# Kernel tuning notes

Measured on AMD Instinct MI355X. Metric: run time of the kernel, lower is better.

Reference implementation:

```python
import jax, jax.numpy as jnp
import numpy as np

N, E, G = 100000, 1600000, 512
D_IN, D_H, D_OUT = 128, 128, 1
EPS = 1e-5


def _gcn_conv(x, W, b, src, dst, n):
    # PyG GCNConv: h = x @ W, add self-loops, symmetric-normalized sum aggregation, bias after.
    h = x @ W
    loop = jnp.arange(n)
    s = jnp.concatenate([src, loop])
    d = jnp.concatenate([dst, loop])
    deg = jax.ops.segment_sum(jnp.ones(s.shape[0], dtype=h.dtype), d, num_segments=n)
    dinv = jnp.where(deg > 0, jax.lax.rsqrt(deg), 0.0)
    norm = dinv[s] * dinv[d]  # [E+N]
    out = jax.ops.segment_sum(h[s] * norm[:, None], d, num_segments=n)
    return out + b


def _bn(x, g, b, m, v):
    # eval-mode BatchNorm1d
    return (x - m) * jax.lax.rsqrt(v + EPS) * g + b


def setup_inputs() -> dict:
    key = jax.random.key(0)
    ks = jax.random.split(key, 24)
    x = jax.random.normal(ks[0], (N, D_IN), dtype=jnp.float32)
    edge_index = jax.random.randint(ks[1], (2, E), 0, N, dtype=jnp.int64)
    batch = (jnp.arange(N, dtype=jnp.int64) * G) // N  # sorted, all graphs non-empty
    inp = {"x": x, "edge_index": edge_index, "batch": batch}
    dims = [(D_IN, D_H), (D_H, D_H), (D_H, D_H)]
    for i, (din, dout) in enumerate(dims):
        sc = 1.0 / np.sqrt(din)
        inp[f"W{i}"] = jax.random.normal(ks[2 + 4 * i], (din, dout), dtype=jnp.float32) * sc
        inp[f"cb{i}"] = jnp.zeros((dout,), dtype=jnp.float32)
        inp[f"g{i}"] = jnp.ones((dout,), dtype=jnp.float32)
        inp[f"bt{i}"] = jnp.zeros((dout,), dtype=jnp.float32)
        inp[f"m{i}"] = jax.random.normal(ks[3 + 4 * i], (dout,), dtype=jnp.float32) * 0.1
        inp[f"v{i}"] = jax.random.uniform(ks[4 + 4 * i], (dout,), dtype=jnp.float32, minval=0.5, maxval=1.5)
    inp["L1w"] = jax.random.normal(ks[15], (2 * D_H, D_H), dtype=jnp.float32) / np.sqrt(2 * D_H)
    inp["L1b"] = jnp.zeros((D_H,), dtype=jnp.float32)
    inp["L2w"] = jax.random.normal(ks[16], (D_H, D_H // 2), dtype=jnp.float32) / np.sqrt(D_H)
    inp["L2b"] = jnp.zeros((D_H // 2,), dtype=jnp.float32)
    inp["L3w"] = jax.random.normal(ks[17], (D_H // 2, D_OUT), dtype=jnp.float32) / np.sqrt(D_H // 2)
    inp["L3b"] = jnp.zeros((D_OUT,), dtype=jnp.float32)
    return inp


def reference(x, edge_index, batch,
              W0, cb0, g0, bt0, m0, v0,
              W1, cb1, g1, bt1, m1, v1,
              W2, cb2, g2, bt2, m2, v2,
              L1w, L1b, L2w, L2b, L3w, L3b):
    src, dst = edge_index[0], edge_index[1]
    Ws = [W0, W1, W2]
    cbs = [cb0, cb1, cb2]
    bns = [(g0, bt0, m0, v0), (g1, bt1, m1, v1), (g2, bt2, m2, v2)]
    for i in range(3):
        x_prev = x
        x = _gcn_conv(x, Ws[i], cbs[i], src, dst, N)
        x = jax.nn.relu(_bn(x, *bns[i]))
        # dropout is identity in eval mode
        if i > 0:
            x = x + x_prev  # residual (shapes match for i > 0)
    ones = jnp.ones((N,), dtype=x.dtype)
    cnt = jax.ops.segment_sum(ones, batch, num_segments=G)[:, None]
    x_mean = jax.ops.segment_sum(x, batch, num_segments=G) / cnt
    x_max = jax.ops.segment_max(x, batch, num_segments=G)
    h = jnp.concatenate([x_mean, x_max], axis=1)  # [G, 2*D_H]
    h = jax.nn.relu(h @ L1w + L1b)
    h = jax.nn.relu(h @ L2w + L2b)
    return h @ L3w + L3b  # [G, 1]
```

## Files before the change

### kernel.cpp

```cpp
#include <hip/hip_runtime.h>
#include <math.h>

#define DH 128
#define EPSB 1e-5f
#define MAXB 832
#define BCAP 3072

typedef __attribute__((ext_vector_type(8))) short short8;
typedef __attribute__((ext_vector_type(4))) float f32x4;

static __device__ __forceinline__ unsigned short f2bf(float f) {
    unsigned u = __float_as_uint(f);
    u += 0x7fffu + ((u >> 16) & 1u);
    return (unsigned short)(u >> 16);
}
static __device__ __forceinline__ float bf2f(unsigned short h) {
    return __uint_as_float(((unsigned)h) << 16);
}


__launch_bounds__(256)
__global__ void k_bucketA(const int* __restrict__ src, const int* __restrict__ dst,
                          int* __restrict__ gcur, int* __restrict__ bbuf,
                          const int* __restrict__ batch, int* __restrict__ starts,
                          int E, int NB, int chunk, int N, int G)
{
    __shared__ int cnt[MAXB];
    __shared__ int base[MAXB];
    const int t = threadIdx.x;

    for (int i = blockIdx.x * 256 + t; i < N; i += gridDim.x * 256) {
        int b = batch[i];
        if (i == 0) { starts[0] = 0; starts[G] = N; }
        else if (batch[i - 1] != b) starts[b] = i;
    }

    for (int i = t; i < NB; i += 256) cnt[i] = 0;
    __syncthreads();
    const int e0 = blockIdx.x * chunk;
    const int e1 = min(E, e0 + chunk);
    for (int e = e0 + t; e < e1; e += 256)
        atomicAdd(&cnt[dst[e] >> 7], 1);
    __syncthreads();
    for (int i = t; i < NB; i += 256) {
        int c = cnt[i];
        base[i] = (c > 0) ? atomicAdd(&gcur[i], c) : 0;
        cnt[i] = 0;
    }
    __syncthreads();
    for (int e = e0 + t; e < e1; e += 256) {
        int d = dst[e];
        int b = d >> 7;
        int o = base[b] + atomicAdd(&cnt[b], 1);
        if (o < BCAP) bbuf[(size_t)b * BCAP + o] = (src[e] << 7) | (d & 127);
    }
}

__launch_bounds__(1024)
__global__ void k_bgscan(const int* __restrict__ gcur, int* __restrict__ bbase,
                         int* __restrict__ rowptr, int NB, int N, int E)
{
    __shared__ int s[1024];
    int t = threadIdx.x;
    int v = (t < NB) ? min(gcur[t], BCAP) : 0;
    s[t] = v;
    __syncthreads();
    for (int off = 1; off < 1024; off <<= 1) {
        int u = (t >= off) ? s[t - off] : 0;
        __syncthreads();
        s[t] += u;
        __syncthreads();
    }
    if (t < NB) bbase[t] = s[t] - v;
    if (t == 0) rowptr[N] = E;
}

__launch_bounds__(256)
__global__ void k_bfinal(const int* __restrict__ gcur, const int* __restrict__ bbase,
                         const int* __restrict__ bbuf, int* __restrict__ rowptr,
                         float* __restrict__ dinv, int* __restrict__ csr_src, int N)
{
    __shared__ int ebuf[BCAP];
    __shared__ int dcnt[128];
    __shared__ int sp[128];
    const int b = blockIdx.x, t = threadIdx.x;
    const int c = min(gcur[b], BCAP);
    const int base = bbase[b];
    const int* p = bbuf + (size_t)b * BCAP;
    for (int i = t; i < c; i += 256) ebuf[i] = p[i];
    if (t < 128) dcnt[t] = 0;
    __syncthreads();
    for (int i = t; i < c; i += 256) atomicAdd(&dcnt[ebuf[i] & 127], 1);
    __syncthreads();
    if (t < 128) sp[t] = dcnt[t];
    __syncthreads();
    for (int off = 1; off < 128; off <<= 1) {
        int u = (t < 128 && t >= off) ? sp[t - off] : 0;
        __syncthreads();
        if (t < 128) sp[t] += u;
        __syncthreads();
    }
    if (t < 128) {
        sp[t] -= dcnt[t];
        int d = b * 128 + t;
        if (d < N) {
            rowptr[d] = base + sp[t];
            dinv[d] = rsqrtf((float)(dcnt[t] + 1));
        }
        dcnt[t] = 0;
    }
    __syncthreads();
    for (int i = t; i < c; i += 256) {
        int e = ebuf[i];
        int dl = e & 127;
        int o = atomicAdd(&dcnt[dl], 1);
        csr_src[base + sp[dl] + o] = e >> 7;
    }
}


__global__ void k_wfrag(const float* __restrict__ W0, const float* __restrict__ W1,
                        const float* __restrict__ W2, unsigned short* __restrict__ Wf0) {
    int fid = blockIdx.x * 4 + (threadIdx.x >> 6);
    int lane = threadIdx.x & 63;
    int l = fid >> 6;
    int f = fid & 63;
    const float* W = (l == 0) ? W0 : (l == 1) ? W1 : W2;
    unsigned short* Wf = Wf0 + (size_t)l * 32768;
    int nt = f & 3, s = (f >> 2) & 3, p = (f >> 4) & 1, nh = f >> 5;
    int n = nh * 64 + nt * 16 + (lane & 15);
    int kbase = s * 32 + (lane >> 4) * 8;
    unsigned short o[8];
#pragma unroll
    for (int j = 0; j < 8; ++j) {
        float w = W[(size_t)(kbase + j) * DH + n];
        unsigned short h = f2bf(w);
        o[j] = p ? f2bf(w - bf2f(h)) : h;
    }
    unsigned short* d = Wf + (size_t)f * 512 + lane * 8;
    *(ushort4*)d       = make_ushort4(o[0], o[1], o[2], o[3]);
    *(ushort4*)(d + 4) = make_ushort4(o[4], o[5], o[6], o[7]);
}


#define LDA0 132

__launch_bounds__(256)
__global__ void k_gemm0(const float* __restrict__ X,
                        const unsigned short* __restrict__ Wf,
                        const float* __restrict__ dinv,
                        unsigned short* __restrict__ hs, int N)
{
    __shared__ float As[64 * LDA0];

    const int tid  = threadIdx.x;
    const int lane = tid & 63, wave = tid >> 6;
    const int mh = wave >> 1, nh = wave & 1;
    const int rowBase = blockIdx.x * 64;
    const int r15 = lane & 15, quad = lane >> 4;

    {
        const float4* gp = (const float4*)(X + (size_t)rowBase * DH);
#pragma unroll
        for (int it = 0; it < 8; ++it) {
            int idx = it * 256 + tid;
            int grow = idx >> 5, gcol = idx & 31;
            float4 v = make_float4(0.f, 0.f, 0.f, 0.f);
            if (rowBase + grow < N) v = gp[idx];
            *(float4*)(As + grow * LDA0 + gcol * 4) = v;
        }
    }
    __syncthreads();

    f32x4 acc[2][4];
#pragma unroll
    for (int mt = 0; mt < 2; ++mt)
#pragma unroll
        for (int nt = 0; nt < 4; ++nt)
            acc[mt][nt] = (f32x4){0.f, 0.f, 0.f, 0.f};

#pragma unroll
    for (int s = 0; s < 4; ++s) {
        short8 wfh[4], wfl[4];
#pragma unroll
        for (int nt = 0; nt < 4; ++nt) {
            wfh[nt] = *(const short8*)(Wf + ((((nh * 2 + 0) * 4 + s) * 4 + nt) * 512) + lane * 8);
            wfl[nt] = *(const short8*)(Wf + ((((nh * 2 + 1) * 4 + s) * 4 + nt) * 512) + lane * 8);
        }
#pragma unroll
        for (int mt = 0; mt < 2; ++mt) {
            const float* ap = As + (mh * 32 + mt * 16 + r15) * LDA0 + s * 32 + quad * 8;
            short8 ah, al;
#pragma unroll
            for (int j = 0; j < 8; ++j) {
                float v = ap[j];
                unsigned short h = f2bf(v);
                ah[j] = (short)h;
                al[j] = (short)f2bf(v - bf2f(h));
            }
#pragma unroll
            for (int nt = 0; nt < 4; ++nt) {
                acc[mt][nt] = __builtin_amdgcn_mfma_f32_16x16x32_bf16(ah, wfh[nt], acc[mt][nt], 0, 0, 0);
                acc[mt][nt] = __builtin_amdgcn_mfma_f32_16x16x32_bf16(ah, wfl[nt], acc[mt][nt], 0, 0, 0);
                acc[mt][nt] = __builtin_amdgcn_mfma_f32_16x16x32_bf16(al, wfh[nt], acc[mt][nt], 0, 0, 0);
            }
        }
    }

#pragma unroll
    for (int mt = 0; mt < 2; ++mt) {
        int rl = mh * 32 + mt * 16 + quad * 4;
#pragma unroll
        for (int reg = 0; reg < 4; ++reg) {
            int row = rowBase + rl + reg;
            if (row < N) {
                float sc = dinv[row];
#pragma unroll
                for (int nt = 0; nt < 4; ++nt)
                    hs[(size_t)row * DH + nh * 64 + nt * 16 + r15] = f2bf(acc[mt][nt][reg] * sc);
            }
        }
    }
}


#define LDAP 136

__launch_bounds__(256)
__global__ void k_gemm_pl(const unsigned short* __restrict__ Xh,
                          const unsigned short* __restrict__ Xl,
                          const unsigned short* __restrict__ Wf,
                          const float* __restrict__ dinv,
                          unsigned short* __restrict__ hs, int N)
{
    __shared__ unsigned short Ah[64 * LDAP];
    __shared__ unsigned short Al[64 * LDAP];

    const int tid  = threadIdx.x;
    const int lane = tid & 63, wave = tid >> 6;
    const int mh = wave >> 1, nh = wave & 1;
    const int rowBase = blockIdx.x * 64;
    const int r15 = lane & 15, quad = lane >> 4;

    {
        const uint4* gh = (const uint4*)(Xh + (size_t)rowBase * DH);
        const uint4* gl = (const uint4*)(Xl + (size_t)rowBase * DH);
#pragma unroll
        for (int it = 0; it < 4; ++it) {
            int idx = it * 256 + tid;
            int grow = idx >> 4, gcol8 = (idx & 15) * 8;
            uint4 vh = make_uint4(0, 0, 0, 0), vl = make_uint4(0, 0, 0, 0);
            if (rowBase + grow < N) { vh = gh[idx]; vl = gl[idx]; }
            *(uint4*)(Ah + grow * LDAP + gcol8) = vh;
            *(uint4*)(Al + grow * LDAP + gcol8) = vl;
        }
    }
    __syncthreads();

    f32x4 acc[2][4];
#pragma unroll
    for (int mt = 0; mt < 2; ++mt)
#pragma unroll
        for (int nt = 0; nt < 4; ++nt)
            acc[mt][nt] = (f32x4){0.f, 0.f, 0.f, 0.f};

#pragma unroll
    for (int s = 0; s < 4; ++s) {
        short8 wfh[4], wfl[4];
#pragma unroll
        for (int nt = 0; nt < 4; ++nt) {
            wfh[nt] = *(const short8*)(Wf + ((((nh * 2 + 0) * 4 + s) * 4 + nt) * 512) + lane * 8);
            wfl[nt] = *(const short8*)(Wf + ((((nh * 2 + 1) * 4 + s) * 4 + nt) * 512) + lane * 8);
        }
#pragma unroll
        for (int mt = 0; mt < 2; ++mt) {
            int arow = mh * 32 + mt * 16 + r15;
            short8 ah = *(const short8*)(Ah + arow * LDAP + s * 32 + quad * 8);
            short8 al = *(const short8*)(Al + arow * LDAP + s * 32 + quad * 8);
#pragma unroll
            for (int nt = 0; nt < 4; ++nt) {
                acc[mt][nt] = __builtin_amdgcn_mfma_f32_16x16x32_bf16(ah, wfh[nt], acc[mt][nt], 0, 0, 0);
                acc[mt][nt] = __builtin_amdgcn_mfma_f32_16x16x32_bf16(ah, wfl[nt], acc[mt][nt], 0, 0, 0);
                acc[mt][nt] = __builtin_amdgcn_mfma_f32_16x16x32_bf16(al, wfh[nt], acc[mt][nt], 0, 0, 0);
            }
        }
    }

#pragma unroll
    for (int mt = 0; mt < 2; ++mt) {
        int rl = mh * 32 + mt * 16 + quad * 4;
#pragma unroll
        for (int reg = 0; reg < 4; ++reg) {
            int row = rowBase + rl + reg;
            if (row < N) {
                float sc = dinv[row];
#pragma unroll
                for (int nt = 0; nt < 4; ++nt)
                    hs[(size_t)row * DH + nh * 64 + nt * 16 + r15] = f2bf(acc[mt][nt][reg] * sc);
            }
        }
    }
}


__launch_bounds__(256)
__global__ void k_gather(const unsigned short* __restrict__ hs, const int* __restrict__ rowptr,
                         const int* __restrict__ csr_src, const float* __restrict__ dinv,
                         const float* __restrict__ cb, const float* __restrict__ bm,
                         const float* __restrict__ bv, const float* __restrict__ bg,
                         const float* __restrict__ bb,
                         const unsigned short* __restrict__ ph,
                         const unsigned short* __restrict__ pl,
                         unsigned short* __restrict__ oh,
                         unsigned short* __restrict__ ol,
                         int N)
{
    const int node = (blockIdx.x * blockDim.x + threadIdx.x) >> 5;
    const int lh = threadIdx.x & 31;
    if (node >= N) return;
    const int f = lh * 4;
    const int e0 = rowptr[node], e1 = rowptr[node + 1];

    ushort4 su = *(const ushort4*)(hs + (size_t)node * DH + f);
    float a0 = bf2f(su.x), a1 = bf2f(su.y), a2 = bf2f(su.z), a3 = bf2f(su.w);

    for (int base = e0; base < e1; base += 32) {
        int cnt = e1 - base; if (cnt > 32) cnt = 32;
        int idx = (lh < cnt) ? csr_src[base + lh] : 0;
        int i = 0;
        for (; i + 4 <= cnt; i += 4) {
            int s0 = __shfl(idx, i,     32), s1 = __shfl(idx, i + 1, 32);
            int s2 = __shfl(idx, i + 2, 32), s3 = __shfl(idx, i + 3, 32);
            ushort4 v0 = *(const ushort4*)(hs + (size_t)s0 * DH + f);
            ushort4 v1 = *(const ushort4*)(hs + (size_t)s1 * DH + f);
            ushort4 v2 = *(const ushort4*)(hs + (size_t)s2 * DH + f);
            ushort4 v3 = *(const ushort4*)(hs + (size_t)s3 * DH + f);
            a0 += (bf2f(v0.x) + bf2f(v1.x)) + (bf2f(v2.x) + bf2f(v3.x));
            a1 += (bf2f(v0.y) + bf2f(v1.y)) + (bf2f(v2.y) + bf2f(v3.y));
            a2 += (bf2f(v0.z) + bf2f(v1.z)) + (bf2f(v2.z) + bf2f(v3.z));
            a3 += (bf2f(v0.w) + bf2f(v1.w)) + (bf2f(v2.w) + bf2f(v3.w));
        }
        for (; i < cnt; ++i) {
            int s = __shfl(idx, i, 32);
            ushort4 v = *(const ushort4*)(hs + (size_t)s * DH + f);
            a0 += bf2f(v.x); a1 += bf2f(v.y); a2 += bf2f(v.z); a3 += bf2f(v.w);
        }
    }

    const float sc = dinv[node];
    const float4 vcb = *(const float4*)(cb + f);
    const float4 vbm = *(const float4*)(bm + f);
    const float4 vbv = *(const float4*)(bv + f);
    const float4 vbg = *(const float4*)(bg + f);
    const float4 vbb = *(const float4*)(bb + f);
    float o0 = (a0 * sc + vcb.x - vbm.x) * rsqrtf(vbv.x + EPSB) * vbg.x + vbb.x;
    float o1 = (a1 * sc + vcb.y - vbm.y) * rsqrtf(vbv.y + EPSB) * vbg.y + vbb.y;
    float o2 = (a2 * sc + vcb.z - vbm.z) * rsqrtf(vbv.z + EPSB) * vbg.z + vbb.z;
    float o3 = (a3 * sc + vcb.w - vbm.w) * rsqrtf(vbv.w + EPSB) * vbg.w + vbb.w;
    o0 = fmaxf(o0, 0.f); o1 = fmaxf(o1, 0.f); o2 = fmaxf(o2, 0.f); o3 = fmaxf(o3, 0.f);
    if (ph) {
        ushort4 hv = *(const ushort4*)(ph + (size_t)node * DH + f);
        ushort4 lv = *(const ushort4*)(pl + (size_t)node * DH + f);
        o0 += bf2f(hv.x) + bf2f(lv.x);
        o1 += bf2f(hv.y) + bf2f(lv.y);
        o2 += bf2f(hv.z) + bf2f(lv.z);
        o3 += bf2f(hv.w) + bf2f(lv.w);
    }
    unsigned short h0 = f2bf(o0), h1 = f2bf(o1), h2 = f2bf(o2), h3 = f2bf(o3);
    *(ushort4*)(oh + (size_t)node * DH + f) = make_ushort4(h0, h1, h2, h3);
    *(ushort4*)(ol + (size_t)node * DH + f) =
        make_ushort4(f2bf(o0 - bf2f(h0)), f2bf(o1 - bf2f(h1)),
                     f2bf(o2 - bf2f(h2)), f2bf(o3 - bf2f(h3)));
}


__launch_bounds__(128)
__global__ void k_pool_mlp(const unsigned short* __restrict__ xh,
                           const unsigned short* __restrict__ xl,
                           const int* __restrict__ starts,
                           const float* __restrict__ L1w, const float* __restrict__ L1b,
                           const float* __restrict__ L2w, const float* __restrict__ L2b,
                           const float* __restrict__ L3w, const float* __restrict__ L3b,
                           float* __restrict__ out)
{
    int g = blockIdx.x, t = threadIdx.x;
    int s0 = starts[g], s1 = starts[g + 1];
    const int half = t >> 6;
    const int tc = t & 63;
    const int fc = tc * 2;

    float sA = 0.f, sB = 0.f;
    float mA = -INFINITY, mB = -INFINITY;
    for (int i = s0 + half; i < s1; i += 2) {
        unsigned hv = *(const unsigned*)(xh + (size_t)i * DH + fc);
        unsigned lv = *(const unsigned*)(xl + (size_t)i * DH + fc);
        float vA = bf2f((unsigned short)hv) + bf2f((unsigned short)lv);
        float vB = bf2f((unsigned short)(hv >> 16)) + bf2f((unsigned short)(lv >> 16));
        sA += vA; sB += vB;
        mA = fmaxf(mA, vA); mB = fmaxf(mB, vB);
    }

    __shared__ float ps[2][128];
    __shared__ float pm[2][128];
    ps[half][fc] = sA; ps[half][fc + 1] = sB;
    pm[half][fc] = mA; pm[half][fc + 1] = mB;
    __syncthreads();

    __shared__ float h[256];
    if (half == 0) {
        float inv = 1.f / (float)(s1 - s0);
        h[fc]     = (ps[0][fc]     + ps[1][fc])     * inv;
        h[fc + 1] = (ps[0][fc + 1] + ps[1][fc + 1]) * inv;
        h[128 + fc]     = fmaxf(pm[0][fc],     pm[1][fc]);
        h[128 + fc + 1] = fmaxf(pm[0][fc + 1], pm[1][fc + 1]);
    }
    __syncthreads();

    float a = L1b[t];
    for (int k = 0; k < 256; ++k) a += h[k] * L1w[k * DH + t];
    __shared__ float h1[128];
    h1[t] = fmaxf(a, 0.f);
    __syncthreads();

    __shared__ float h2[64];
    if (t < 64) {
        float a2 = L2b[t];
        for (int k = 0; k < 128; ++k) a2 += h1[k] * L2w[k * 64 + t];
        h2[t] = fmaxf(a2, 0.f);
    }
    __syncthreads();

    if (t < 64) {
        float p = h2[t] * L3w[t];
#pragma unroll
        for (int off = 32; off > 0; off >>= 1) p += __shfl_down(p, off, 64);
        if (t == 0) out[g] = p + L3b[0];
    }
}


static inline char* align16(char* p) {
    return (char*)(((uintptr_t)p + 15) & ~(uintptr_t)15);
}

extern "C" void kernel_launch(void* const* d_in, const int* in_sizes, int n_in,
                              void* d_out, int out_size, void* d_ws, size_t ws_size,
                              hipStream_t stream)
{
    const float* x     = (const float*)d_in[0];
    const int*   ei    = (const int*)d_in[1];
    const int*   batch = (const int*)d_in[2];
    const int N = in_sizes[0] / DH;
    const int E = in_sizes[1] / 2;
    const int G = out_size;
    const int* src = ei;
    const int* dst = ei + E;

    const float* W[3]  = {(const float*)d_in[3],  (const float*)d_in[9],  (const float*)d_in[15]};
    const float* cb[3] = {(const float*)d_in[4],  (const float*)d_in[10], (const float*)d_in[16]};
    const float* bg[3] = {(const float*)d_in[5],  (const float*)d_in[11], (const float*)d_in[17]};
    const float* bt[3] = {(const float*)d_in[6],  (const float*)d_in[12], (const float*)d_in[18]};
    const float* bm[3] = {(const float*)d_in[7],  (const float*)d_in[13], (const float*)d_in[19]};
    const float* bv[3] = {(const float*)d_in[8],  (const float*)d_in[14], (const float*)d_in[20]};
    const float* L1w = (const float*)d_in[21]; const float* L1b = (const float*)d_in[22];
    const float* L2w = (const float*)d_in[23]; const float* L2b = (const float*)d_in[24];
    const float* L3w = (const float*)d_in[25]; const float* L3b = (const float*)d_in[26];

    char* wsp = (char*)d_ws;
    size_t planeB = (size_t)N * DH * sizeof(unsigned short);
    unsigned short* HS  = (unsigned short*)wsp; wsp += planeB;
    unsigned short* AH  = (unsigned short*)wsp; wsp += planeB;
    unsigned short* AL  = (unsigned short*)wsp; wsp += planeB;
    unsigned short* BH  = (unsigned short*)wsp; wsp += planeB;
    unsigned short* BL  = (unsigned short*)wsp; wsp += planeB;
    unsigned short* Wfrag = (unsigned short*)wsp; wsp += 3 * 65536;
    float* dinv   = (float*)wsp; wsp += (size_t)N * sizeof(float);
    int*   rowptr = (int*)wsp;   wsp = align16(wsp + (size_t)(N + 1) * sizeof(int));
    int*   csr_src= (int*)wsp;   wsp += (size_t)E * sizeof(int);
    int*   starts = (int*)wsp;   wsp = align16(wsp + (size_t)(G + 1) * sizeof(int));
    int*   gcur   = (int*)wsp;   wsp = align16(wsp + (size_t)MAXB * sizeof(int));
    int*   bbase  = (int*)wsp;   wsp = align16(wsp + (size_t)MAXB * sizeof(int));
    int*   bbuf   = (int*)wsp;   wsp += (size_t)MAXB * BCAP * sizeof(int);

    const int NB = (N + 127) >> 7;
    const int nblkA = 128;
    const int chunk = (E + nblkA - 1) / nblkA;

    hipMemsetAsync(gcur, 0, (size_t)NB * sizeof(int), stream);
    k_bucketA<<<nblkA, 256, 0, stream>>>(src, dst, gcur, bbuf, batch, starts,
                                         E, NB, chunk, N, G);
    k_bgscan <<<1, 1024, 0, stream>>>(gcur, bbase, rowptr, NB, N, E);
    k_bfinal <<<NB, 256, 0, stream>>>(gcur, bbase, bbuf, rowptr, dinv, csr_src, N);
    k_wfrag  <<<48, 256, 0, stream>>>(W[0], W[1], W[2], Wfrag);

    int gemmGrid = (N + 63) / 64;
    int gathGrid = ((size_t)N * 32 + 255) / 256;

    k_gemm0<<<gemmGrid, 256, 0, stream>>>(x, Wfrag, dinv, HS, N);
    k_gather<<<gathGrid, 256, 0, stream>>>(HS, rowptr, csr_src, dinv,
                                           cb[0], bm[0], bv[0], bg[0], bt[0],
                                           nullptr, nullptr, AH, AL, N);
    k_gemm_pl<<<gemmGrid, 256, 0, stream>>>(AH, AL, Wfrag + 32768, dinv, HS, N);
    k_gather<<<gathGrid, 256, 0, stream>>>(HS, rowptr, csr_src, dinv,
                                           cb[1], bm[1], bv[1], bg[1], bt[1],
                                           AH, AL, BH, BL, N);
    k_gemm_pl<<<gemmGrid, 256, 0, stream>>>(BH, BL, Wfrag + 65536, dinv, HS, N);
    k_gather<<<gathGrid, 256, 0, stream>>>(HS, rowptr, csr_src, dinv,
                                           cb[2], bm[2], bv[2], bg[2], bt[2],
                                           BH, BL, AH, AL, N);

    k_pool_mlp<<<G, 128, 0, stream>>>(AH, AL, starts, L1w, L1b, L2w, L2b, L3w, L3b,
                                      (float*)d_out);
}
```

Baseline: 530.1 us.

## Widen gather loads to 16 bytes per lane, use more pool threads and bucket blocks

The gather kernel now assigns 16 lanes per node, each loading 8 bf16 features with one 128-bit load instead of 32 lanes with 64-bit loads. This halves the load instructions and shuffles per edge and lets each wave process twice as many nodes. The pool/MLP kernel moves from 128 to 256 threads so four row groups reduce each graph, and the bucketing kernel launches 512 blocks instead of 128. Each lane now holds more accumulator registers, and the shorter edge chunks of 16 mean more loop iterations per node.

Result: faster. 507.4 us (-4.3%).

```diff
diff --git a/kernel.cpp b/kernel.cpp
--- a/kernel.cpp
+++ b/kernel.cpp
@@ -17,6 +17,8 @@
 static __device__ __forceinline__ float bf2f(unsigned short h) {
     return __uint_as_float(((unsigned)h) << 16);
 }
+static __device__ __forceinline__ float blo(unsigned u) { return __uint_as_float(u << 16); }
+static __device__ __forceinline__ float bhi(unsigned u) { return __uint_as_float(u & 0xFFFF0000u); }
 
 
 __launch_bounds__(256)
@@ -315,66 +317,84 @@
                          unsigned short* __restrict__ ol,
                          int N)
 {
-    const int node = (blockIdx.x * blockDim.x + threadIdx.x) >> 5;
-    const int lh = threadIdx.x & 31;
+    const int node = (blockIdx.x * blockDim.x + threadIdx.x) >> 4;
+    const int lh = threadIdx.x & 15;
     if (node >= N) return;
-    const int f = lh * 4;
+    const int f = lh * 8;
     const int e0 = rowptr[node], e1 = rowptr[node + 1];
 
-    ushort4 su = *(const ushort4*)(hs + (size_t)node * DH + f);
-    float a0 = bf2f(su.x), a1 = bf2f(su.y), a2 = bf2f(su.z), a3 = bf2f(su.w);
-
-    for (int base = e0; base < e1; base += 32) {
-        int cnt = e1 - base; if (cnt > 32) cnt = 32;
+    const uint4* hsv = (const uint4*)hs;
+    float a[8];
+    {
+        uint4 sv = hsv[(size_t)node * 16 + lh];
+        a[0] = blo(sv.x); a[1] = bhi(sv.x); a[2] = blo(sv.y); a[3] = bhi(sv.y);
+        a[4] = blo(sv.z); a[5] = bhi(sv.z); a[6] = blo(sv.w); a[7] = bhi(sv.w);
+    }
+
+    for (int base = e0; base < e1; base += 16) {
+        int cnt = e1 - base; if (cnt > 16) cnt = 16;
         int idx = (lh < cnt) ? csr_src[base + lh] : 0;
         int i = 0;
         for (; i + 4 <= cnt; i += 4) {
-            int s0 = __shfl(idx, i,     32), s1 = __shfl(idx, i + 1, 32);
-            int s2 = __shfl(idx, i + 2, 32), s3 = __shfl(idx, i + 3, 32);
-            ushort4 v0 = *(const ushort4*)(hs + (size_t)s0 * DH + f);
-            ushort4 v1 = *(const ushort4*)(hs + (size_t)s1 * DH + f);
-            ushort4 v2 = *(const ushort4*)(hs + (size_t)s2 * DH + f);
-            ushort4 v3 = *(const ushort4*)(hs + (size_t)s3 * DH + f);
-            a0 += (bf2f(v0.x) + bf2f(v1.x)) + (bf2f(v2.x) + bf2f(v3.x));
-            a1 += (bf2f(v0.y) + bf2f(v1.y)) + (bf2f(v2.y) + bf2f(v3.y));
-            a2 += (bf2f(v0.z) + bf2f(v1.z)) + (bf2f(v2.z) + bf2f(v3.z));
-            a3 += (bf2f(v0.w) + bf2f(v1.w)) + (bf2f(v2.w) + bf2f(v3.w));
+            int s0 = __shfl(idx, i,     16), s1 = __shfl(idx, i + 1, 16);
+            int s2 = __shfl(idx, i + 2, 16), s3 = __shfl(idx, i + 3, 16);
+            uint4 v0 = hsv[(size_t)s0 * 16 + lh];
+            uint4 v1 = hsv[(size_t)s1 * 16 + lh];
+            uint4 v2 = hsv[(size_t)s2 * 16 + lh];
+            uint4 v3 = hsv[(size_t)s3 * 16 + lh];
+            a[0] += (blo(v0.x) + blo(v1.x)) + (blo(v2.x) + blo(v3.x));
+            a[1] += (bhi(v0.x) + bhi(v1.x)) + (bhi(v2.x) + bhi(v3.x));
+            a[2] += (blo(v0.y) + blo(v1.y)) + (blo(v2.y) + blo(v3.y));
+            a[3] += (bhi(v0.y) + bhi(v1.y)) + (bhi(v2.y) + bhi(v3.y));
+            a[4] += (blo(v0.z) + blo(v1.z)) + (blo(v2.z) + blo(v3.z));
+            a[5] += (bhi(v0.z) + bhi(v1.z)) + (bhi(v2.z) + bhi(v3.z));
+            a[6] += (blo(v0.w) + blo(v1.w)) + (blo(v2.w) + blo(v3.w));
+            a[7] += (bhi(v0.w) + bhi(v1.w)) + (bhi(v2.w) + bhi(v3.w));
         }
         for (; i < cnt; ++i) {
-            int s = __shfl(idx, i, 32);
-            ushort4 v = *(const ushort4*)(hs + (size_t)s * DH + f);
-            a0 += bf2f(v.x); a1 += bf2f(v.y); a2 += bf2f(v.z); a3 += bf2f(v.w);
+            int s = __shfl(idx, i, 16);
+            uint4 v = hsv[(size_t)s * 16 + lh];
+            a[0] += blo(v.x); a[1] += bhi(v.x); a[2] += blo(v.y); a[3] += bhi(v.y);
+            a[4] += blo(v.z); a[5] += bhi(v.z); a[6] += blo(v.w); a[7] += bhi(v.w);
         }
     }
 
     const float sc = dinv[node];
-    const float4 vcb = *(const float4*)(cb + f);
-    const float4 vbm = *(const float4*)(bm + f);
-    const float4 vbv = *(const float4*)(bv + f);
-    const float4 vbg = *(const float4*)(bg + f);
-    const float4 vbb = *(const float4*)(bb + f);
-    float o0 = (a0 * sc + vcb.x - vbm.x) * rsqrtf(vbv.x + EPSB) * vbg.x + vbb.x;
-    float o1 = (a1 * sc + vcb.y - vbm.y) * rsqrtf(vbv.y + EPSB) * vbg.y + vbb.y;
-    float o2 = (a2 * sc + vcb.z - vbm.z) * rsqrtf(vbv.z + EPSB) * vbg.z + vbb.z;
-    float o3 = (a3 * sc + vcb.w - vbm.w) * rsqrtf(vbv.w + EPSB) * vbg.w + vbb.w;
-    o0 = fmaxf(o0, 0.f); o1 = fmaxf(o1, 0.f); o2 = fmaxf(o2, 0.f); o3 = fmaxf(o3, 0.f);
+    float cbv[8], bmv[8], bvv[8], bgv[8], bbv[8];
+    *(float4*)cbv = *(const float4*)(cb + f); *(float4*)(cbv + 4) = *(const float4*)(cb + f + 4);
+    *(float4*)bmv = *(const float4*)(bm + f); *(float4*)(bmv + 4) = *(const float4*)(bm + f + 4);
+    *(float4*)bvv = *(const float4*)(bv + f); *(float4*)(bvv + 4) = *(const float4*)(bv + f + 4);
+    *(float4*)bgv = *(const float4*)(bg + f); *(float4*)(bgv + 4) = *(const float4*)(bg + f + 4);
+    *(float4*)bbv = *(const float4*)(bb + f); *(float4*)(bbv + 4) = *(const float4*)(bb + f + 4);
+
+    float o[8];
+#pragma unroll
+    for (int j = 0; j < 8; ++j) {
+        float v = (a[j] * sc + cbv[j] - bmv[j]) * rsqrtf(bvv[j] + EPSB) * bgv[j] + bbv[j];
+        o[j] = fmaxf(v, 0.f);
+    }
     if (ph) {
-        ushort4 hv = *(const ushort4*)(ph + (size_t)node * DH + f);
-        ushort4 lv = *(const ushort4*)(pl + (size_t)node * DH + f);
-        o0 += bf2f(hv.x) + bf2f(lv.x);
-        o1 += bf2f(hv.y) + bf2f(lv.y);
-        o2 += bf2f(hv.z) + bf2f(lv.z);
-        o3 += bf2f(hv.w) + bf2f(lv.w);
-    }
-    unsigned short h0 = f2bf(o0), h1 = f2bf(o1), h2 = f2bf(o2), h3 = f2bf(o3);
-    *(ushort4*)(oh + (size_t)node * DH + f) = make_ushort4(h0, h1, h2, h3);
-    *(ushort4*)(ol + (size_t)node * DH + f) =
-        make_ushort4(f2bf(o0 - bf2f(h0)), f2bf(o1 - bf2f(h1)),
-                     f2bf(o2 - bf2f(h2)), f2bf(o3 - bf2f(h3)));
-}
-
-
-__launch_bounds__(128)
+        uint4 hv = *(const uint4*)(ph + (size_t)node * DH + f);
+        uint4 lv = *(const uint4*)(pl + (size_t)node * DH + f);
+        o[0] += blo(hv.x) + blo(lv.x); o[1] += bhi(hv.x) + bhi(lv.x);
+        o[2] += blo(hv.y) + blo(lv.y); o[3] += bhi(hv.y) + bhi(lv.y);
+        o[4] += blo(hv.z) + blo(lv.z); o[5] += bhi(hv.z) + bhi(lv.z);
+        o[6] += blo(hv.w) + blo(lv.w); o[7] += bhi(hv.w) + bhi(lv.w);
+    }
+    unsigned hw[4], lw[4];
+#pragma unroll
+    for (int p = 0; p < 4; ++p) {
+        unsigned short hA = f2bf(o[2 * p]), hB = f2bf(o[2 * p + 1]);
+        hw[p] = (unsigned)hA | ((unsigned)hB << 16);
+        lw[p] = (unsigned)f2bf(o[2 * p] - bf2f(hA)) |
+                ((unsigned)f2bf(o[2 * p + 1] - bf2f(hB)) << 16);
+    }
+    *(uint4*)(oh + (size_t)node * DH + f) = make_uint4(hw[0], hw[1], hw[2], hw[3]);
+    *(uint4*)(ol + (size_t)node * DH + f) = make_uint4(lw[0], lw[1], lw[2], lw[3]);
+}
+
+
+__launch_bounds__(256)
 __global__ void k_pool_mlp(const unsigned short* __restrict__ xh,
                            const unsigned short* __restrict__ xl,
                            const int* __restrict__ starts,
@@ -385,41 +405,45 @@
 {
     int g = blockIdx.x, t = threadIdx.x;
     int s0 = starts[g], s1 = starts[g + 1];
-    const int half = t >> 6;
+    const int rg = t >> 6;
     const int tc = t & 63;
     const int fc = tc * 2;
 
     float sA = 0.f, sB = 0.f;
     float mA = -INFINITY, mB = -INFINITY;
-    for (int i = s0 + half; i < s1; i += 2) {
+    for (int i = s0 + rg; i < s1; i += 4) {
         unsigned hv = *(const unsigned*)(xh + (size_t)i * DH + fc);
         unsigned lv = *(const unsigned*)(xl + (size_t)i * DH + fc);
-        float vA = bf2f((unsigned short)hv) + bf2f((unsigned short)lv);
-        float vB = bf2f((unsigned short)(hv >> 16)) + bf2f((unsigned short)(lv >> 16));
+        float vA = blo(hv) + blo(lv);
+        float vB = bhi(hv) + bhi(lv);
         sA += vA; sB += vB;
         mA = fmaxf(mA, vA); mB = fmaxf(mB, vB);
     }
 
-    __shared__ float ps[2][128];
-    __shared__ float pm[2][128];
-    ps[half][fc] = sA; ps[half][fc + 1] = sB;
-    pm[half][fc] = mA; pm[half][fc + 1] = mB;
+    __shared__ float ps[4][128];
+    __shared__ float pm[4][128];
+    ps[rg][fc] = sA; ps[rg][fc + 1] = sB;
+    pm[rg][fc] = mA; pm[rg][fc + 1] = mB;
     __syncthreads();
 
     __shared__ float h[256];
-    if (half == 0) {
+    if (rg == 0) {
         float inv = 1.f / (float)(s1 - s0);
-        h[fc]     = (ps[0][fc]     + ps[1][fc])     * inv;
-        h[fc + 1] = (ps[0][fc + 1] + ps[1][fc + 1]) * inv;
-        h[128 + fc]     = fmaxf(pm[0][fc],     pm[1][fc]);
-        h[128 + fc + 1] = fmaxf(pm[0][fc + 1], pm[1][fc + 1]);
-    }
-    __syncthreads();
-
-    float a = L1b[t];
-    for (int k = 0; k < 256; ++k) a += h[k] * L1w[k * DH + t];
+#pragma unroll
+        for (int j = 0; j < 2; ++j) {
+            int fi = fc + j;
+            h[fi] = ((ps[0][fi] + ps[1][fi]) + (ps[2][fi] + ps[3][fi])) * inv;
+            h[128 + fi] = fmaxf(fmaxf(pm[0][fi], pm[1][fi]), fmaxf(pm[2][fi], pm[3][fi]));
+        }
+    }
+    __syncthreads();
+
     __shared__ float h1[128];
-    h1[t] = fmaxf(a, 0.f);
+    if (t < 128) {
+        float a = L1b[t];
+        for (int k = 0; k < 256; ++k) a += h[k] * L1w[k * DH + t];
+        h1[t] = fmaxf(a, 0.f);
+    }
     __syncthreads();
 
     __shared__ float h2[64];
@@ -483,7 +507,7 @@
     int*   bbuf   = (int*)wsp;   wsp += (size_t)MAXB * BCAP * sizeof(int);
 
     const int NB = (N + 127) >> 7;
-    const int nblkA = 128;
+    const int nblkA = 512;
     const int chunk = (E + nblkA - 1) / nblkA;
 
     hipMemsetAsync(gcur, 0, (size_t)NB * sizeof(int), stream);
@@ -494,7 +518,7 @@
     k_wfrag  <<<48, 256, 0, stream>>>(W[0], W[1], W[2], Wfrag);
 
     int gemmGrid = (N + 63) / 64;
-    int gathGrid = ((size_t)N * 32 + 255) / 256;
+    int gathGrid = ((size_t)N * 16 + 255) / 256;
 
     k_gemm0<<<gemmGrid, 256, 0, stream>>>(x, Wfrag, dinv, HS, N);
     k_gather<<<gathGrid, 256, 0, stream>>>(HS, rowptr, csr_src, dinv,
@@ -509,6 +533,6 @@
                                            cb[2], bm[2], bv[2], bg[2], bt[2],
                                            BH, BL, AH, AL, N);
 
-    k_pool_mlp<<<G, 128, 0, stream>>>(AH, AL, starts, L1w, L1b, L2w, L2b, L3w, L3b,
+    k_pool_mlp<<<G, 256, 0, stream>>>(AH, AL, starts, L1w, L1b, L2w, L2b, L3w, L3b,
                                       (float*)d_out);
 }
```
